# Kernel optimization log

Hardware: AMD Instinct MI355X
Metric: run time of the kernel (lower is better)

Reference implementation:

```python
import jax, jax.numpy as jnp
import numpy as np

H, D = 4, 32  # num_heads, per-head out dim (out_feats=128)
N_AGENT, N_GT, N_UAV = 50000, 50000, 50000
E = 600000
IN = 64


def _gat(x_src, x_dst, src, dst, W_src, W_dst, al, ar, W_res, b, num_dst):
    """DGL-style bipartite GATConv with residual, bias and ReLU activation."""
    fs = (x_src @ W_src).reshape(-1, H, D)      # [Ns,H,D]
    fd = (x_dst @ W_dst).reshape(-1, H, D)      # [Nd,H,D]
    el = jnp.sum(fs * al, axis=-1)              # [Ns,H]
    er = jnp.sum(fd * ar, axis=-1)              # [Nd,H]
    e = jax.nn.leaky_relu(el[src] + er[dst], 0.2)          # [E,H]
    # segment softmax over incoming edges of each dst node
    emax = jax.ops.segment_max(e, dst, num_segments=num_dst)   # [Nd,H], -inf for deg-0
    ee = jnp.exp(e - emax[dst])
    denom = jax.ops.segment_sum(ee, dst, num_segments=num_dst)
    a = ee / denom[dst]                          # [E,H]
    msg = fs[src] * a[:, :, None]                # [E,H,D]
    rst = jax.ops.segment_sum(msg, dst, num_segments=num_dst)  # [Nd,H,D]; zeros for deg-0
    res = (x_dst @ W_res).reshape(-1, H, D)      # residual projection
    out = jax.nn.relu(rst + res + b.reshape(1, H, D))
    return out.reshape(num_dst, H * D)


def setup_inputs() -> dict:
    key = jax.random.key(0)
    ks = jax.random.split(key, 20)
    s = 0.1  # weight init scale
    return {
        'x_gt': jax.random.normal(ks[0], (N_GT, IN), jnp.float32),
        'x_uav': jax.random.normal(ks[1], (N_UAV, IN), jnp.float32),
        'x_agent': jax.random.normal(ks[2], (N_AGENT, IN), jnp.float32),
        'src_gt': jax.random.randint(ks[3], (E,), 0, N_GT, jnp.int32),
        'dst_gt': jax.random.randint(ks[4], (E,), 0, N_AGENT, jnp.int32),
        'src_uav': jax.random.randint(ks[5], (E,), 0, N_UAV, jnp.int32),
        'dst_uav': jax.random.randint(ks[6], (E,), 0, N_AGENT, jnp.int32),
        'W_src_gt': s * jax.random.normal(ks[7], (IN, H * D), jnp.float32),
        'W_dst_gt': s * jax.random.normal(ks[8], (IN, H * D), jnp.float32),
        'attn_l_gt': s * jax.random.normal(ks[9], (H, D), jnp.float32),
        'attn_r_gt': s * jax.random.normal(ks[10], (H, D), jnp.float32),
        'W_res_gt': s * jax.random.normal(ks[11], (IN, H * D), jnp.float32),
        'b_gt': jnp.zeros((H * D,), jnp.float32),
        'W_src_uav': s * jax.random.normal(ks[12], (IN, H * D), jnp.float32),
        'W_dst_uav': s * jax.random.normal(ks[13], (IN, H * D), jnp.float32),
        'attn_l_uav': s * jax.random.normal(ks[14], (H, D), jnp.float32),
        'attn_r_uav': s * jax.random.normal(ks[15], (H, D), jnp.float32),
        'W_res_uav': s * jax.random.normal(ks[16], (IN, H * D), jnp.float32),
        'b_uav': jnp.zeros((H * D,), jnp.float32),
        'W_f': s * jax.random.normal(ks[17], (2 * H * D, H * D), jnp.float32),
        'b_f': jnp.zeros((H * D,), jnp.float32),
    }


def reference(x_gt, x_uav, x_agent, src_gt, dst_gt, src_uav, dst_uav,
              W_src_gt, W_dst_gt, attn_l_gt, attn_r_gt, W_res_gt, b_gt,
              W_src_uav, W_dst_uav, attn_l_uav, attn_r_uav, W_res_uav, b_uav,
              W_f, b_f):
    h_gt = _gat(x_gt, x_agent, src_gt, dst_gt, W_src_gt, W_dst_gt,
                attn_l_gt, attn_r_gt, W_res_gt, b_gt, N_AGENT)
    h_uav = _gat(x_uav, x_agent, src_uav, dst_uav, W_src_uav, W_dst_uav,
                 attn_l_uav, attn_r_uav, W_res_uav, b_uav, N_AGENT)
    h = jnp.concatenate([h_gt, h_uav], axis=1)   # [N_agent, 256]
    return jax.nn.relu(h @ W_f + b_f)            # [N_agent, 128]
```

## Files before the change

### kernel.cpp

```cpp
#include <hip/hip_runtime.h>
#include <hip/hip_bf16.h>

using bf16 = __hip_bfloat16;

#define NA 50000
#define NE 600000

typedef __attribute__((ext_vector_type(8))) short short8;
typedef __attribute__((ext_vector_type(4))) float f32x4;

#define HBUF_B   0u
#define FS_B     25600000u
#define EL_B     51200000u
#define RECS_B   54400000u
#define CNT_B    73600000u
#define ROW_B    74000000u
#define TOPS_B   74400016u
#define FLAG_B   74400528u
#define WST_GT_B 74400544u
#define WST_UAV_B 74416928u
#define WRT_B    74433312u
#define WFT_B    74466080u
#define ELT_GT_B 74531616u
#define ELT_UAV_B 74533664u
#define ERT_B    74535712u
#define RANK_B   74537760u
#define WS_BYTES 79337760u

__device__ __forceinline__ float b2f(bf16 v) { return __bfloat162float(v); }

__device__ __forceinline__ float ldf(const void* p, size_t i, int f32) {
    return f32 ? ((const float*)p)[i] : b2f(((const bf16*)p)[i]);
}

__device__ __forceinline__ unsigned short f2bs(float v) {
    bf16 t = __float2bfloat16(v);
    return *(unsigned short*)&t;
}

__device__ __forceinline__ float lrelu_exp(float v) {
    v = v > 0.f ? v : 0.2f * v;
    return __expf(v);
}

__device__ __forceinline__ unsigned int pack_bf16x2(float a, float b) {
    return (unsigned int)f2bs(a) | ((unsigned int)f2bs(b) << 16);
}

__device__ __forceinline__ float lo_f(unsigned int u) { return __uint_as_float(u << 16); }
__device__ __forceinline__ float hi_f(unsigned int u) { return __uint_as_float(u & 0xffff0000u); }

__device__ __forceinline__ short8 ldfrag8(const void* p, size_t off, int f32) {
    if (!f32) return *(const short8*)((const unsigned short*)p + off);
    union { short8 s; unsigned int u[4]; } r;
    const float* fp = (const float*)p + off;
#pragma unroll
    for (int j = 0; j < 4; ++j) r.u[j] = pack_bf16x2(fp[2 * j], fp[2 * j + 1]);
    return r.s;
}

__device__ int probe_f32(const void* x0) {
    __shared__ int cnt;
    if (threadIdx.x == 0) cnt = 0;
    __syncthreads();
    const bf16* p = (const bf16*)x0;
    int bad = 0;
    for (int i = threadIdx.x; i < 1024; i += 256) {
        float av = fabsf(b2f(p[i]));
        if (!(av <= 1e6f)) bad++;
    }
    if (bad) atomicAdd(&cnt, bad);
    __syncthreads();
    return cnt > 8;
}

__global__ void HeteroVisionConv_29703993819529_kernel(
    const void* x0,
    const void* Wsg, const void* alg, const void* Wdg, const void* arg_,
    const void* Wsu, const void* alu, const void* Wdu, const void* aru,
    const void* Wrg, const void* Wru, const void* Wf,
    const int* dg, const int* du, unsigned int* cnt, unsigned int* rank,
    unsigned short* wsT_gt, unsigned short* wsT_uav, unsigned short* wrT,
    unsigned short* wfT, unsigned short* elT_gt, unsigned short* elT_uav,
    unsigned short* erT,
    int* flag, unsigned int* outp, long sent) {
    int b = blockIdx.x, t = threadIdx.x;
    if (b >= 21) {
        int idx = (b - 21) * 256 + t;
        if (idx >= 300000) return;
        int g = idx >= 150000;
        int e = (idx - g * 150000) * 4;
        int4 d4 = *(const int4*)((g ? du : dg) + e);
        unsigned int* c = cnt + g * NA;
        uint4 r4;
        r4.x = atomicAdd(&c[d4.x], 1u);
        r4.y = atomicAdd(&c[d4.y], 1u);
        r4.z = atomicAdd(&c[d4.z], 1u);
        r4.w = atomicAdd(&c[d4.w], 1u);
        *(uint4*)(rank + (size_t)g * NE + e) = r4;
        return;
    }
    int f32 = probe_f32(x0);
    if (b == 20) {
        if (t == 0) { flag[0] = f32; outp[sent] = 0x447A447Au; }
        return;
    }
    if (b < 8) {
        for (int i = t; i < 16 * 256; i += 256) {
            int n = b * 16 + (i >> 8), k = i & 255;
            wfT[n * 256 + k] = f2bs(ldf(Wf, (size_t)k * 128 + n, f32));
        }
    } else if (b < 12) {
        for (int i = t; i < 64 * 64; i += 256) {
            int n = (b - 8) * 64 + (i >> 6), k = i & 63;
            float v = (n < 128) ? ldf(Wrg, (size_t)k * 128 + n, f32)
                                : ldf(Wru, (size_t)k * 128 + (n - 128), f32);
            wrT[n * 64 + k] = f2bs(v);
        }
    } else if (b < 14) {
        for (int i = t; i < 64 * 64; i += 256) {
            int n = (b - 12) * 64 + (i >> 6), k = i & 63;
            wsT_gt[n * 64 + k] = f2bs(ldf(Wsg, (size_t)k * 128 + n, f32));
        }
    } else if (b < 16) {
        for (int i = t; i < 64 * 64; i += 256) {
            int n = (b - 14) * 64 + (i >> 6), k = i & 63;
            wsT_uav[n * 64 + k] = f2bs(ldf(Wsu, (size_t)k * 128 + n, f32));
        }
    } else {
        int m = b - 16;
        const void* Wm = (m == 0) ? Wsg : (m == 1) ? Wdg : (m == 2) ? Wsu : Wdu;
        const void* Am = (m == 0) ? alg : (m == 1) ? arg_ : (m == 2) ? alu : aru;
        int k = t >> 2, h = t & 3;
        float a = 0.f;
        for (int d = 0; d < 32; ++d)
            a += ldf(Wm, (size_t)k * 128 + h * 32 + d, f32) *
                 ldf(Am, (size_t)h * 32 + d, f32);
        unsigned short v = f2bs(a);
        if (m == 0) {
            elT_gt[h * 64 + k] = v;
            for (int i = t; i < 12 * 64; i += 256) elT_gt[(4 + (i >> 6)) * 64 + (i & 63)] = 0;
        } else if (m == 2) {
            elT_uav[h * 64 + k] = v;
            for (int i = t; i < 12 * 64; i += 256) elT_uav[(4 + (i >> 6)) * 64 + (i & 63)] = 0;
        } else if (m == 1) {
            erT[h * 64 + k] = v;
        } else {
            erT[(4 + h) * 64 + k] = v;
            for (int i = t; i < 8 * 64; i += 256) erT[(8 + (i >> 6)) * 64 + (i & 63)] = 0;
        }
    }
}

__global__ void node_fs_k(const void* xg, const void* xu,
                          const unsigned short* wsT_gt, const unsigned short* wsT_uav,
                          const unsigned short* elT_gt, const unsigned short* elT_uav,
                          float* elbase, bf16* fs, const int* flag) {
    int f32 = *flag;
    int bx = blockIdx.x, g = bx / 782, b = bx % 782;
    const void* A = g ? xu : xg;
    const unsigned short* WT = g ? wsT_uav : wsT_gt;
    const unsigned short* ET = g ? elT_uav : elT_gt;
    float* elout = elbase + (g ? 400000 : 0);
    bf16* out = fs + (size_t)g * NA * 128;
    __shared__ unsigned short Bt[128 * 72];
    int t = threadIdx.x;
    for (int i = t * 8; i < 128 * 64; i += 256 * 8) {
        short8 v = *(const short8*)(WT + i);
        int n = i >> 6, k = i & 63;
        *(short8*)&Bt[n * 72 + k] = v;
    }
    __syncthreads();
    int lane = t & 63, w = t >> 6;
    int m = lane & 15, quad = lane >> 4;
    int row = b * 64 + w * 16 + m;
    int rowc = row < NA ? row : NA - 1;
    short8 a0 = ldfrag8(A, (size_t)rowc * 64 + quad * 8, f32);
    short8 a1 = ldfrag8(A, (size_t)rowc * 64 + 32 + quad * 8, f32);
    f32x4 acc[8];
#pragma unroll
    for (int nt = 0; nt < 8; ++nt) acc[nt] = (f32x4){0.f, 0.f, 0.f, 0.f};
#pragma unroll
    for (int nt = 0; nt < 8; ++nt) {
        short8 b0 = *(const short8*)&Bt[(nt * 16 + m) * 72 + quad * 8];
        short8 b1 = *(const short8*)&Bt[(nt * 16 + m) * 72 + 32 + quad * 8];
        acc[nt] = __builtin_amdgcn_mfma_f32_16x16x32_bf16(a0, b0, acc[nt], 0, 0, 0);
        acc[nt] = __builtin_amdgcn_mfma_f32_16x16x32_bf16(a1, b1, acc[nt], 0, 0, 0);
    }
    f32x4 eacc = (f32x4){0.f, 0.f, 0.f, 0.f};
    {
        short8 e0 = *(const short8*)&ET[m * 64 + quad * 8];
        short8 e1 = *(const short8*)&ET[m * 64 + 32 + quad * 8];
        eacc = __builtin_amdgcn_mfma_f32_16x16x32_bf16(a0, e0, eacc, 0, 0, 0);
        eacc = __builtin_amdgcn_mfma_f32_16x16x32_bf16(a1, e1, eacc, 0, 0, 0);
    }
    int srow = b * 64 + w * 16 + quad * 4;
#pragma unroll
    for (int nt = 0; nt < 8; ++nt) {
#pragma unroll
        for (int r = 0; r < 4; ++r) {
            int rr = srow + r;
            if (rr < NA) out[(size_t)rr * 128 + nt * 16 + m] = __float2bfloat16(acc[nt][r]);
        }
    }
    if (m < 4) {
#pragma unroll
        for (int r = 0; r < 4; ++r) {
            int rr = srow + r;
            if (rr < NA) elout[(size_t)rr * 4 + m] = eacc[r];
        }
    }
}

__global__ void res_k(const void* xa, const unsigned short* wrT,
                      const unsigned short* erT,
                      const void* bg, const void* bu,
                      float* elbase, bf16* hbuf, const int* flag) {
    int f32 = *flag;
    int b = blockIdx.x;
    __shared__ unsigned short Bt[256 * 72];
    __shared__ float bl[256];
    int t = threadIdx.x;
    for (int i = t * 8; i < 256 * 64; i += 256 * 8) {
        short8 v = *(const short8*)(wrT + i);
        int n = i >> 6, k = i & 63;
        *(short8*)&Bt[n * 72 + k] = v;
    }
    bl[t] = (t < 128) ? ldf(bg, t, f32) : ldf(bu, t - 128, f32);
    __syncthreads();
    int lane = t & 63, w = t >> 6;
    int m = lane & 15, quad = lane >> 4;
    int row = b * 64 + w * 16 + m;
    int rowc = row < NA ? row : NA - 1;
    short8 a0 = ldfrag8(xa, (size_t)rowc * 64 + quad * 8, f32);
    short8 a1 = ldfrag8(xa, (size_t)rowc * 64 + 32 + quad * 8, f32);
    f32x4 acc[16];
#pragma unroll
    for (int nt = 0; nt < 16; ++nt) acc[nt] = (f32x4){0.f, 0.f, 0.f, 0.f};
#pragma unroll
    for (int nt = 0; nt < 16; ++nt) {
        short8 b0 = *(const short8*)&Bt[(nt * 16 + m) * 72 + quad * 8];
        short8 b1 = *(const short8*)&Bt[(nt * 16 + m) * 72 + 32 + quad * 8];
        acc[nt] = __builtin_amdgcn_mfma_f32_16x16x32_bf16(a0, b0, acc[nt], 0, 0, 0);
        acc[nt] = __builtin_amdgcn_mfma_f32_16x16x32_bf16(a1, b1, acc[nt], 0, 0, 0);
    }
    f32x4 eacc = (f32x4){0.f, 0.f, 0.f, 0.f};
    {
        short8 e0 = *(const short8*)&erT[m * 64 + quad * 8];
        short8 e1 = *(const short8*)&erT[m * 64 + 32 + quad * 8];
        eacc = __builtin_amdgcn_mfma_f32_16x16x32_bf16(a0, e0, eacc, 0, 0, 0);
        eacc = __builtin_amdgcn_mfma_f32_16x16x32_bf16(a1, e1, eacc, 0, 0, 0);
    }
    int srow = b * 64 + w * 16 + quad * 4;
#pragma unroll
    for (int nt = 0; nt < 16; ++nt) {
        int col = nt * 16 + m;
#pragma unroll
        for (int r = 0; r < 4; ++r) {
            int rr = srow + r;
            if (rr < NA)
                hbuf[(size_t)rr * 256 + col] = __float2bfloat16(acc[nt][r] + bl[col]);
        }
    }
    if (m < 8) {
        float* ero = (m < 4) ? (elbase + 200000) : (elbase + 600000);
        int mm = m & 3;
#pragma unroll
        for (int r = 0; r < 4; ++r) {
            int rr = srow + r;
            if (rr < NA) ero[(size_t)rr * 4 + mm] = eacc[r];
        }
    }
}

__global__ void scan1_k(const unsigned int* cnt, unsigned int* row, unsigned int* tops) {
    __shared__ unsigned int sh[256];
    int b = blockIdx.x, t = threadIdx.x;
    int base = b * 1024 + t * 4;
    unsigned int v[4];
    for (int j = 0; j < 4; ++j) v[j] = (base + j < 100000) ? cnt[base + j] : 0u;
    unsigned int s = v[0] + v[1] + v[2] + v[3];
    sh[t] = s;
    __syncthreads();
    for (int off = 1; off < 256; off <<= 1) {
        unsigned int x = (t >= off) ? sh[t - off] : 0u;
        __syncthreads();
        sh[t] += x;
        __syncthreads();
    }
    unsigned int run = sh[t] - s;
    for (int j = 0; j < 4; ++j) {
        if (base + j < 100000) row[base + j] = run;
        run += v[j];
    }
    if (t == 255) tops[b] = sh[255];
}

__global__ void scan2_k(unsigned int* tops, unsigned int* row) {
    __shared__ unsigned int sh[128];
    int t = threadIdx.x;
    unsigned int v = (t < 98) ? tops[t] : 0u;
    sh[t] = v;
    __syncthreads();
    for (int off = 1; off < 128; off <<= 1) {
        unsigned int x = (t >= off) ? sh[t - off] : 0u;
        __syncthreads();
        sh[t] += x;
        __syncthreads();
    }
    if (t < 98) tops[t] = sh[t] - v;
    if (t == 97) row[100000] = sh[97];
}

__global__ void scan3_k(unsigned int* row, const unsigned int* tops) {
    int b = blockIdx.x, t = threadIdx.x;
    unsigned int off = tops[b];
    for (int i = b * 1024 + t; i < b * 1024 + 1024; i += 256) {
        if (i < 100000) row[i] += off;
    }
}

__global__ void scatter_k(const int* sg, const int* dg, const int* su, const int* du,
                          const float* elbase, const unsigned int* row,
                          const unsigned int* rank, uint4* recs) {
    int idx = blockIdx.x * 256 + threadIdx.x;
    if (idx >= 2 * NE) return;
    int g = idx >= NE;
    int e = idx - g * NE;
    int s = (g ? su : sg)[e];
    int d = (g ? du : dg)[e];
    const float4* el4 = (const float4*)(elbase + (g ? 400000 : 0));
    const float4* er4 = (const float4*)(elbase + (g ? 600000 : 200000));
    unsigned int pos = row[g * NA + d] + rank[idx];
    float4 l = el4[s], r = er4[d];
    uint4 rec;
    rec.x = (unsigned int)s;
    rec.y = pack_bf16x2(lrelu_exp(l.x + r.x), lrelu_exp(l.y + r.y));
    rec.z = pack_bf16x2(lrelu_exp(l.z + r.z), lrelu_exp(l.w + r.w));
    rec.w = 0u;
    recs[pos] = rec;
}

__global__ void gather_k(const unsigned int* row, const uint4* recs,
                         const bf16* fs, bf16* hbuf) {
    int wid = (blockIdx.x * 256 + threadIdx.x) >> 6;
    int lane = threadIdx.x & 63;
    if (wid >= 2 * NA) return;
    int g = wid / NA, d = wid - g * NA;
    int eg = lane >> 4;
    int cl = lane & 15;
    int hsel = cl >> 3;
    int hodd = (cl >> 2) & 1;
    unsigned int start = row[g * NA + d];
    unsigned int end   = row[g * NA + d + 1];
    const uint4* fs4 = (const uint4*)(fs + (size_t)g * NA * 128);

    float denom = 0.f;
    float a[8];
#pragma unroll
    for (int k = 0; k < 8; ++k) a[k] = 0.f;

    if (start < end) {
        uint4 rr[4], rn[4];
#pragma unroll
        for (int j = 0; j < 4; ++j) {
            unsigned int idx = start + 4 * j + eg;
            rr[j] = recs[idx < end ? idx : end - 1];
        }
        for (unsigned int i = start; i < end; i += 16) {
            uint4 uu[4];
#pragma unroll
            for (int j = 0; j < 4; ++j) uu[j] = fs4[(size_t)rr[j].x * 16 + cl];
            unsigned int inext = i + 16;
#pragma unroll
            for (int j = 0; j < 4; ++j) {
                unsigned int idx = inext + 4 * j + eg;
                rn[j] = recs[idx < end ? idx : end - 1];
            }
#pragma unroll
            for (int j = 0; j < 4; ++j) {
                unsigned int idx = i + 4 * j + eg;
                unsigned int pp = hsel ? rr[j].z : rr[j].y;
                float e = hodd ? hi_f(pp) : lo_f(pp);
                if (idx >= end) e = 0.f;
                denom += e;
                a[0] += lo_f(uu[j].x) * e;
                a[1] += hi_f(uu[j].x) * e;
                a[2] += lo_f(uu[j].y) * e;
                a[3] += hi_f(uu[j].y) * e;
                a[4] += lo_f(uu[j].z) * e;
                a[5] += hi_f(uu[j].z) * e;
                a[6] += lo_f(uu[j].w) * e;
                a[7] += hi_f(uu[j].w) * e;
            }
#pragma unroll
            for (int j = 0; j < 4; ++j) rr[j] = rn[j];
        }
    }
#pragma unroll
    for (int k = 0; k < 8; ++k) {
        a[k] += __shfl_xor(a[k], 16, 64);
        a[k] += __shfl_xor(a[k], 32, 64);
    }
    denom += __shfl_xor(denom, 16, 64);
    denom += __shfl_xor(denom, 32, 64);
    if (lane < 16) {
        float inv = (end > start) ? 1.f / denom : 0.f;
        uint4* hp = (uint4*)(hbuf + (size_t)d * 256 + g * 128) + cl;
        uint4 rv = *hp;
        float v0 = a[0] * inv + lo_f(rv.x);
        float v1 = a[1] * inv + hi_f(rv.x);
        float v2 = a[2] * inv + lo_f(rv.y);
        float v3 = a[3] * inv + hi_f(rv.y);
        float v4 = a[4] * inv + lo_f(rv.z);
        float v5 = a[5] * inv + hi_f(rv.z);
        float v6 = a[6] * inv + lo_f(rv.w);
        float v7 = a[7] * inv + hi_f(rv.w);
        v0 = v0 > 0.f ? v0 : 0.f;
        v1 = v1 > 0.f ? v1 : 0.f;
        v2 = v2 > 0.f ? v2 : 0.f;
        v3 = v3 > 0.f ? v3 : 0.f;
        v4 = v4 > 0.f ? v4 : 0.f;
        v5 = v5 > 0.f ? v5 : 0.f;
        v6 = v6 > 0.f ? v6 : 0.f;
        v7 = v7 > 0.f ? v7 : 0.f;
        uint4 o;
        o.x = pack_bf16x2(v0, v1);
        o.y = pack_bf16x2(v2, v3);
        o.z = pack_bf16x2(v4, v5);
        o.w = pack_bf16x2(v6, v7);
        *hp = o;
    }
}

__global__ void final_k(const bf16* hbuf, const unsigned short* wfT,
                        const void* bfp, void* outp, const int* flag) {
    int f32 = *flag;
    int b = blockIdx.x;
    __shared__ unsigned short Bt[128 * 72];
    __shared__ float bl[128];
    int t = threadIdx.x;
    if (t < 128) bl[t] = ldf(bfp, t, f32);
    int lane = t & 63, w = t >> 6;
    int m = lane & 15, quad = lane >> 4;
    int row = b * 64 + w * 16 + m;
    int rowc = row < NA ? row : NA - 1;
    f32x4 acc[8];
#pragma unroll
    for (int nt = 0; nt < 8; ++nt) acc[nt] = (f32x4){0.f, 0.f, 0.f, 0.f};
    for (int kc = 0; kc < 4; ++kc) {
        __syncthreads();
        for (int i = t * 8; i < 128 * 64; i += 256 * 8) {
            int n = i >> 6, k = i & 63;
            short8 v = *(const short8*)(wfT + (size_t)n * 256 + kc * 64 + k);
            *(short8*)&Bt[n * 72 + k] = v;
        }
        __syncthreads();
        short8 a0 = *(const short8*)((const unsigned short*)hbuf +
                                     (size_t)rowc * 256 + kc * 64 + quad * 8);
        short8 a1 = *(const short8*)((const unsigned short*)hbuf +
                                     (size_t)rowc * 256 + kc * 64 + 32 + quad * 8);
#pragma unroll
        for (int nt = 0; nt < 8; ++nt) {
            short8 b0 = *(const short8*)&Bt[(nt * 16 + m) * 72 + quad * 8];
            short8 b1 = *(const short8*)&Bt[(nt * 16 + m) * 72 + 32 + quad * 8];
            acc[nt] = __builtin_amdgcn_mfma_f32_16x16x32_bf16(a0, b0, acc[nt], 0, 0, 0);
            acc[nt] = __builtin_amdgcn_mfma_f32_16x16x32_bf16(a1, b1, acc[nt], 0, 0, 0);
        }
    }
    int srow = b * 64 + w * 16 + quad * 4;
#pragma unroll
    for (int nt = 0; nt < 8; ++nt) {
        int col = nt * 16 + m;
        float bv = bl[col];
#pragma unroll
        for (int r = 0; r < 4; ++r) {
            int rr = srow + r;
            if (rr < NA) {
                float v = acc[nt][r] + bv;
                v = v > 0.f ? v : 0.f;
                if (f32) ((float*)outp)[(size_t)rr * 128 + col] = v;
                else ((bf16*)outp)[(size_t)rr * 128 + col] = __float2bfloat16(v);
            }
        }
    }
}

extern "C" void kernel_launch(void* const* d_in, const int* in_sizes, int n_in,
                              void* d_out, int out_size, void* d_ws, size_t ws_size,
                              hipStream_t stream) {
    const void* x_gt     = d_in[0];
    const void* x_uav    = d_in[1];
    const void* x_ag     = d_in[2];
    const int*  src_gt   = (const int*)d_in[3];
    const int*  dst_gt   = (const int*)d_in[4];
    const int*  src_uav  = (const int*)d_in[5];
    const int*  dst_uav  = (const int*)d_in[6];
    const void* Wsrc_gt  = d_in[7];
    const void* Wdst_gt  = d_in[8];
    const void* al_gt    = d_in[9];
    const void* ar_gt    = d_in[10];
    const void* Wres_gt  = d_in[11];
    const void* b_gt     = d_in[12];
    const void* Wsrc_uav = d_in[13];
    const void* Wdst_uav = d_in[14];
    const void* al_uav   = d_in[15];
    const void* ar_uav   = d_in[16];
    const void* Wres_uav = d_in[17];
    const void* b_uav    = d_in[18];
    const void* W_f      = d_in[19];
    const void* b_f      = d_in[20];

    char* wsb = (char*)d_ws;
    bf16* hbuf = (bf16*)(wsb + HBUF_B);
    bf16* fs = (bf16*)(wsb + FS_B);
    float* el = (float*)(wsb + EL_B);
    uint4* recs = (uint4*)(wsb + RECS_B);
    unsigned int* cnt = (unsigned int*)(wsb + CNT_B);
    unsigned int* row = (unsigned int*)(wsb + ROW_B);
    unsigned int* tops = (unsigned int*)(wsb + TOPS_B);
    int* flag = (int*)(wsb + FLAG_B);
    unsigned short* wsT_gt = (unsigned short*)(wsb + WST_GT_B);
    unsigned short* wsT_uav = (unsigned short*)(wsb + WST_UAV_B);
    unsigned short* wrT = (unsigned short*)(wsb + WRT_B);
    unsigned short* wfT = (unsigned short*)(wsb + WFT_B);
    unsigned short* elT_gt = (unsigned short*)(wsb + ELT_GT_B);
    unsigned short* elT_uav = (unsigned short*)(wsb + ELT_UAV_B);
    unsigned short* erT = (unsigned short*)(wsb + ERT_B);
    unsigned int* rank = (unsigned int*)(wsb + RANK_B);

    if (ws_size < (size_t)WS_BYTES) {
        hipMemsetAsync(d_out, 0x42, (size_t)out_size * 2, stream);
        return;
    }

    long sent = (long)out_size / 2 - 1;

    hipMemsetAsync(cnt, 0, 100000 * 4, stream);
    HeteroVisionConv_29703993819529_kernel<<<21 + 1172, 256, 0, stream>>>(
        x_gt, Wsrc_gt, al_gt, Wdst_gt, ar_gt, Wsrc_uav, al_uav, Wdst_uav, ar_uav,
        Wres_gt, Wres_uav, W_f, dst_gt, dst_uav, cnt, rank,
        wsT_gt, wsT_uav, wrT, wfT, elT_gt, elT_uav, erT,
        flag, (unsigned int*)d_out, sent);
    node_fs_k<<<1564, 256, 0, stream>>>(x_gt, x_uav, wsT_gt, wsT_uav,
                                        elT_gt, elT_uav, el, fs, flag);
    res_k<<<782, 256, 0, stream>>>(x_ag, wrT, erT, b_gt, b_uav, el, hbuf, flag);
    scan1_k<<<98, 256, 0, stream>>>(cnt, row, tops);
    scan2_k<<<1, 128, 0, stream>>>(tops, row);
    scan3_k<<<98, 256, 0, stream>>>(row, tops);
    scatter_k<<<4688, 256, 0, stream>>>(src_gt, dst_gt, src_uav, dst_uav,
                                        el, row, rank, recs);
    gather_k<<<25000, 256, 0, stream>>>(row, recs, fs, hbuf);
    final_k<<<782, 256, 0, stream>>>(hbuf, wfT, b_f, d_out, flag);
}
```

Baseline: 303.0 us.

## Fuse degree counting, source projection and residual GEMM into one interleaved launch

```diff
diff --git a/kernel.cpp b/kernel.cpp
--- a/kernel.cpp
+++ b/kernel.cpp
@@ -79,27 +79,11 @@
     const void* Wsg, const void* alg, const void* Wdg, const void* arg_,
     const void* Wsu, const void* alu, const void* Wdu, const void* aru,
     const void* Wrg, const void* Wru, const void* Wf,
-    const int* dg, const int* du, unsigned int* cnt, unsigned int* rank,
     unsigned short* wsT_gt, unsigned short* wsT_uav, unsigned short* wrT,
     unsigned short* wfT, unsigned short* elT_gt, unsigned short* elT_uav,
     unsigned short* erT,
     int* flag, unsigned int* outp, long sent) {
     int b = blockIdx.x, t = threadIdx.x;
-    if (b >= 21) {
-        int idx = (b - 21) * 256 + t;
-        if (idx >= 300000) return;
-        int g = idx >= 150000;
-        int e = (idx - g * 150000) * 4;
-        int4 d4 = *(const int4*)((g ? du : dg) + e);
-        unsigned int* c = cnt + g * NA;
-        uint4 r4;
-        r4.x = atomicAdd(&c[d4.x], 1u);
-        r4.y = atomicAdd(&c[d4.y], 1u);
-        r4.z = atomicAdd(&c[d4.z], 1u);
-        r4.w = atomicAdd(&c[d4.w], 1u);
-        *(uint4*)(rank + (size_t)g * NE + e) = r4;
-        return;
-    }
     int f32 = probe_f32(x0);
     if (b == 20) {
         if (t == 0) { flag[0] = f32; outp[sent] = 0x447A447Au; }
@@ -152,75 +136,91 @@
     }
 }
 
-__global__ void node_fs_k(const void* xg, const void* xu,
-                          const unsigned short* wsT_gt, const unsigned short* wsT_uav,
-                          const unsigned short* elT_gt, const unsigned short* elT_uav,
-                          float* elbase, bf16* fs, const int* flag) {
+__global__ void fused_k(const int* dg, const int* du,
+                        unsigned int* cnt, unsigned int* rank,
+                        const void* xg, const void* xu, const void* xa,
+                        const unsigned short* wsT_gt, const unsigned short* wsT_uav,
+                        const unsigned short* elT_gt, const unsigned short* elT_uav,
+                        const unsigned short* wrT, const unsigned short* erT,
+                        const void* bg, const void* bu,
+                        float* elbase, bf16* fs, bf16* hbuf, const int* flag) {
+    __shared__ unsigned short Bt[256 * 72];
+    __shared__ float bl[256];
+    int b = blockIdx.x, t = threadIdx.x;
+
+    if (b < 3516 && (b % 3) == 0) {
+        int idx = (b / 3) * 256 + t;
+        if (idx >= 300000) return;
+        int g = idx >= 150000;
+        int e = (idx - g * 150000) * 4;
+        int4 d4 = *(const int4*)((g ? du : dg) + e);
+        unsigned int* c = cnt + g * NA;
+        uint4 r4;
+        r4.x = atomicAdd(&c[d4.x], 1u);
+        r4.y = atomicAdd(&c[d4.y], 1u);
+        r4.z = atomicAdd(&c[d4.z], 1u);
+        r4.w = atomicAdd(&c[d4.w], 1u);
+        *(uint4*)(rank + (size_t)g * NE + e) = r4;
+        return;
+    }
+    int nidx = (b < 3516) ? (b - b / 3 - 1) : (2344 + (b - 3516));
     int f32 = *flag;
-    int bx = blockIdx.x, g = bx / 782, b = bx % 782;
-    const void* A = g ? xu : xg;
-    const unsigned short* WT = g ? wsT_uav : wsT_gt;
-    const unsigned short* ET = g ? elT_uav : elT_gt;
-    float* elout = elbase + (g ? 400000 : 0);
-    bf16* out = fs + (size_t)g * NA * 128;
-    __shared__ unsigned short Bt[128 * 72];
-    int t = threadIdx.x;
-    for (int i = t * 8; i < 128 * 64; i += 256 * 8) {
-        short8 v = *(const short8*)(WT + i);
-        int n = i >> 6, k = i & 63;
-        *(short8*)&Bt[n * 72 + k] = v;
-    }
-    __syncthreads();
     int lane = t & 63, w = t >> 6;
     int m = lane & 15, quad = lane >> 4;
-    int row = b * 64 + w * 16 + m;
-    int rowc = row < NA ? row : NA - 1;
-    short8 a0 = ldfrag8(A, (size_t)rowc * 64 + quad * 8, f32);
-    short8 a1 = ldfrag8(A, (size_t)rowc * 64 + 32 + quad * 8, f32);
-    f32x4 acc[8];
-#pragma unroll
-    for (int nt = 0; nt < 8; ++nt) acc[nt] = (f32x4){0.f, 0.f, 0.f, 0.f};
-#pragma unroll
-    for (int nt = 0; nt < 8; ++nt) {
-        short8 b0 = *(const short8*)&Bt[(nt * 16 + m) * 72 + quad * 8];
-        short8 b1 = *(const short8*)&Bt[(nt * 16 + m) * 72 + 32 + quad * 8];
-        acc[nt] = __builtin_amdgcn_mfma_f32_16x16x32_bf16(a0, b0, acc[nt], 0, 0, 0);
-        acc[nt] = __builtin_amdgcn_mfma_f32_16x16x32_bf16(a1, b1, acc[nt], 0, 0, 0);
-    }
-    f32x4 eacc = (f32x4){0.f, 0.f, 0.f, 0.f};
-    {
-        short8 e0 = *(const short8*)&ET[m * 64 + quad * 8];
-        short8 e1 = *(const short8*)&ET[m * 64 + 32 + quad * 8];
-        eacc = __builtin_amdgcn_mfma_f32_16x16x32_bf16(a0, e0, eacc, 0, 0, 0);
-        eacc = __builtin_amdgcn_mfma_f32_16x16x32_bf16(a1, e1, eacc, 0, 0, 0);
-    }
-    int srow = b * 64 + w * 16 + quad * 4;
-#pragma unroll
-    for (int nt = 0; nt < 8; ++nt) {
-#pragma unroll
-        for (int r = 0; r < 4; ++r) {
-            int rr = srow + r;
-            if (rr < NA) out[(size_t)rr * 128 + nt * 16 + m] = __float2bfloat16(acc[nt][r]);
-        }
-    }
-    if (m < 4) {
-#pragma unroll
-        for (int r = 0; r < 4; ++r) {
-            int rr = srow + r;
-            if (rr < NA) elout[(size_t)rr * 4 + m] = eacc[r];
-        }
-    }
-}
-
-__global__ void res_k(const void* xa, const unsigned short* wrT,
-                      const unsigned short* erT,
-                      const void* bg, const void* bu,
-                      float* elbase, bf16* hbuf, const int* flag) {
-    int f32 = *flag;
-    int b = blockIdx.x;
-    __shared__ unsigned short Bt[256 * 72];
-    __shared__ float bl[256];
-    int t = threadIdx.x;
+
+    if (nidx < 1564) {
+        int g = nidx / 782, bb = nidx % 782;
+        const void* A = g ? xu : xg;
+        const unsigned short* WT = g ? wsT_uav : wsT_gt;
+        const unsigned short* ET = g ? elT_uav : elT_gt;
+        float* elout = elbase + (g ? 400000 : 0);
+        bf16* out = fs + (size_t)g * NA * 128;
+        for (int i = t * 8; i < 128 * 64; i += 256 * 8) {
+            short8 v = *(const short8*)(WT + i);
+            int n = i >> 6, k = i & 63;
+            *(short8*)&Bt[n * 72 + k] = v;
+        }
+        __syncthreads();
+        int row = bb * 64 + w * 16 + m;
+        int rowc = row < NA ? row : NA - 1;
+        short8 a0 = ldfrag8(A, (size_t)rowc * 64 + quad * 8, f32);
+        short8 a1 = ldfrag8(A, (size_t)rowc * 64 + 32 + quad * 8, f32);
+        f32x4 acc[8];
+#pragma unroll
+        for (int nt = 0; nt < 8; ++nt) acc[nt] = (f32x4){0.f, 0.f, 0.f, 0.f};
+#pragma unroll
+        for (int nt = 0; nt < 8; ++nt) {
+            short8 b0 = *(const short8*)&Bt[(nt * 16 + m) * 72 + quad * 8];
+            short8 b1 = *(const short8*)&Bt[(nt * 16 + m) * 72 + 32 + quad * 8];
+            acc[nt] = __builtin_amdgcn_mfma_f32_16x16x32_bf16(a0, b0, acc[nt], 0, 0, 0);
+            acc[nt] = __builtin_amdgcn_mfma_f32_16x16x32_bf16(a1, b1, acc[nt], 0, 0, 0);
+        }
+        f32x4 eacc = (f32x4){0.f, 0.f, 0.f, 0.f};
+        {
+            short8 e0 = *(const short8*)&ET[m * 64 + quad * 8];
+            short8 e1 = *(const short8*)&ET[m * 64 + 32 + quad * 8];
+            eacc = __builtin_amdgcn_mfma_f32_16x16x32_bf16(a0, e0, eacc, 0, 0, 0);
+            eacc = __builtin_amdgcn_mfma_f32_16x16x32_bf16(a1, e1, eacc, 0, 0, 0);
+        }
+        int srow = bb * 64 + w * 16 + quad * 4;
+#pragma unroll
+        for (int nt = 0; nt < 8; ++nt) {
+#pragma unroll
+            for (int r = 0; r < 4; ++r) {
+                int rr = srow + r;
+                if (rr < NA) out[(size_t)rr * 128 + nt * 16 + m] = __float2bfloat16(acc[nt][r]);
+            }
+        }
+        if (m < 4) {
+#pragma unroll
+            for (int r = 0; r < 4; ++r) {
+                int rr = srow + r;
+                if (rr < NA) elout[(size_t)rr * 4 + m] = eacc[r];
+            }
+        }
+        return;
+    }
+    int bb = nidx - 1564;
     for (int i = t * 8; i < 256 * 64; i += 256 * 8) {
         short8 v = *(const short8*)(wrT + i);
         int n = i >> 6, k = i & 63;
@@ -228,9 +228,7 @@
     }
     bl[t] = (t < 128) ? ldf(bg, t, f32) : ldf(bu, t - 128, f32);
     __syncthreads();
-    int lane = t & 63, w = t >> 6;
-    int m = lane & 15, quad = lane >> 4;
-    int row = b * 64 + w * 16 + m;
+    int row = bb * 64 + w * 16 + m;
     int rowc = row < NA ? row : NA - 1;
     short8 a0 = ldfrag8(xa, (size_t)rowc * 64 + quad * 8, f32);
     short8 a1 = ldfrag8(xa, (size_t)rowc * 64 + 32 + quad * 8, f32);
@@ -251,7 +249,7 @@
         eacc = __builtin_amdgcn_mfma_f32_16x16x32_bf16(a0, e0, eacc, 0, 0, 0);
         eacc = __builtin_amdgcn_mfma_f32_16x16x32_bf16(a1, e1, eacc, 0, 0, 0);
     }
-    int srow = b * 64 + w * 16 + quad * 4;
+    int srow = bb * 64 + w * 16 + quad * 4;
 #pragma unroll
     for (int nt = 0; nt < 16; ++nt) {
         int col = nt * 16 + m;
@@ -537,14 +535,16 @@
     long sent = (long)out_size / 2 - 1;
 
     hipMemsetAsync(cnt, 0, 100000 * 4, stream);
-    HeteroVisionConv_29703993819529_kernel<<<21 + 1172, 256, 0, stream>>>(
+    HeteroVisionConv_29703993819529_kernel<<<21, 256, 0, stream>>>(
         x_gt, Wsrc_gt, al_gt, Wdst_gt, ar_gt, Wsrc_uav, al_uav, Wdst_uav, ar_uav,
-        Wres_gt, Wres_uav, W_f, dst_gt, dst_uav, cnt, rank,
+        Wres_gt, Wres_uav, W_f,
         wsT_gt, wsT_uav, wrT, wfT, elT_gt, elT_uav, erT,
         flag, (unsigned int*)d_out, sent);
-    node_fs_k<<<1564, 256, 0, stream>>>(x_gt, x_uav, wsT_gt, wsT_uav,
-                                        elT_gt, elT_uav, el, fs, flag);
-    res_k<<<782, 256, 0, stream>>>(x_ag, wrT, erT, b_gt, b_uav, el, hbuf, flag);
+    fused_k<<<3518, 256, 0, stream>>>(dst_gt, dst_uav, cnt, rank,
+                                      x_gt, x_uav, x_ag,
+                                      wsT_gt, wsT_uav, elT_gt, elT_uav,
+                                      wrT, erT, b_gt, b_uav,
+                                      el, fs, hbuf, flag);
     scan1_k<<<98, 256, 0, stream>>>(cnt, row, tops);
     scan2_k<<<1, 128, 0, stream>>>(tops, row);
     scan3_k<<<98, 256, 0, stream>>>(row, tops);
```

Result: no change. 298.0 us (-1.6%).
